# Performance work log

Measured on AMD Instinct MI355X. Metric: run time of the kernel, lower is better.

## Reference

```python
import jax, jax.numpy as jnp
import numpy as np

N_NODES = 100000
N_EDGES = 1600000
IN_CH = 128
HID = 128
N_REL = 8


def setup_inputs() -> dict:
    key = jax.random.key(0)
    k_x, k_src, k_dst, k_et, k_w, k_root, k_b = jax.random.split(key, 7)
    x = jax.random.normal(k_x, (N_NODES, IN_CH), dtype=jnp.float32)
    src = jax.random.randint(k_src, (N_EDGES,), 0, N_NODES)
    dst = jax.random.randint(k_dst, (N_EDGES,), 0, N_NODES)
    edge_index = jnp.stack([src, dst], axis=0)  # [2, E]
    edge_type = jax.random.randint(k_et, (N_EDGES,), 0, N_REL)
    # RGCNConv parameters: per-relation weight, root (self-loop) weight, bias
    scale = 1.0 / np.sqrt(IN_CH)
    W = jax.random.normal(k_w, (N_REL, IN_CH, HID), dtype=jnp.float32) * scale
    root = jax.random.normal(k_root, (IN_CH, HID), dtype=jnp.float32) * scale
    bias = jnp.zeros((HID,), dtype=jnp.float32)
    return {"x": x, "edge_index": edge_index, "edge_type": edge_type,
            "W": W, "root": root, "bias": bias}


def reference(x, edge_index, edge_type, W, root, bias):
    # RGCNConv (mean aggregation per relation) + ReLU. Dropout is identity (eval mode).
    # Aggregate-then-transform: mathematically identical to PyG's
    # transform-then-aggregate since the relation transform is linear,
    # but far cheaper (R matmuls over N nodes instead of E edges).
    N = x.shape[0]
    n_rel = W.shape[0]
    src, dst = edge_index[0], edge_index[1]
    x_src = x[src]  # [E, C] gathered neighbor features
    out = x @ root + bias  # root / self-loop term
    for r in range(n_rel):
        mask = (edge_type == r)
        xm = jnp.where(mask[:, None], x_src, 0.0)  # zero out other relations
        agg = jax.ops.segment_sum(xm, dst, num_segments=N)  # [N, C]
        cnt = jax.ops.segment_sum(mask.astype(x.dtype), dst, num_segments=N)
        mean_agg = agg / jnp.maximum(cnt, 1.0)[:, None]
        out = out + mean_agg @ W[r]
    return jax.nn.relu(out)
```

## Files before the change

kernel.cpp:

```cpp
#include <hip/hip_runtime.h>

#define NREL 8
#define CH   128
#define YW   1152
#define YWD  (YW / 2)
#define NCB  9

#define SCAN_ITEMS   16
#define SCAN_THREADS 256
#define SCAN_CHUNK   (SCAN_ITEMS * SCAN_THREADS)
#define SCAN_SHIFT   12

typedef short  short8v __attribute__((ext_vector_type(8)));
typedef float  f32x4   __attribute__((ext_vector_type(4)));

__device__ __forceinline__ unsigned short f2bf(float f) {
    union { float f; unsigned u; } v; v.f = f;
    return (unsigned short)((v.u + 0x7FFFu + ((v.u >> 16) & 1u)) >> 16);
}
__device__ __forceinline__ float lof(unsigned u) {
    union { unsigned u; float f; } v; v.u = u << 16; return v.f;
}
__device__ __forceinline__ float hif(unsigned u) {
    union { unsigned u; float f; } v; v.u = u & 0xFFFF0000u; return v.f;
}
__device__ __forceinline__ void gload_lds16(const void* g, void* l) {
    __builtin_amdgcn_global_load_lds(
        (const __attribute__((address_space(1))) unsigned int*)g,
        (__attribute__((address_space(3))) unsigned int*)l, 16, 0, 0);
}

__global__ __launch_bounds__(256) void bt2_kernel(
    const float* __restrict__ W, const float* __restrict__ root,
    unsigned short* __restrict__ Bt2)
{
    int idx = blockIdx.x * blockDim.x + threadIdx.x;
    if (idx >= YW * CH) return;
    int rc = idx >> 7, k = idx & 127;
    int r = rc >> 7, c = rc & 127;
    float v = (r < NREL) ? W[(size_t)(r * CH + k) * CH + c]
                         : root[(size_t)k * CH + c];
    Bt2[idx] = f2bf(v);
}

__global__ __launch_bounds__(256) void hist_kernel(
    const int* __restrict__ dst, const int* __restrict__ et,
    int* __restrict__ hist, int E)
{
    int e = blockIdx.x * blockDim.x + threadIdx.x;
    if (e < E) atomicAdd(&hist[dst[e] * NREL + et[e]], 1);
}

__global__ __launch_bounds__(SCAN_THREADS) void scan1_kernel(
    const int* __restrict__ hist, int* __restrict__ ofs,
    int* __restrict__ partials, int S)
{
    __shared__ int lds[SCAN_THREADS];
    int t = threadIdx.x;
    int base = blockIdx.x * SCAN_CHUNK + t * SCAN_ITEMS;
    int v[SCAN_ITEMS];
    int s = 0;
#pragma unroll
    for (int j = 0; j < SCAN_ITEMS; j++) {
        int idx = base + j;
        int h = (idx < S) ? hist[idx] : 0;
        v[j] = s; s += h;
    }
    int run = s;
    lds[t] = run; __syncthreads();
    for (int off = 1; off < SCAN_THREADS; off <<= 1) {
        int y = (t >= off) ? lds[t - off] : 0;
        __syncthreads();
        run += y; lds[t] = run; __syncthreads();
    }
    int tb = run - s;
    if (t == SCAN_THREADS - 1) partials[blockIdx.x] = run;
#pragma unroll
    for (int j = 0; j < SCAN_ITEMS; j++) {
        int idx = base + j;
        if (idx < S) ofs[idx] = tb + v[j];
    }
}

__global__ __launch_bounds__(SCAN_THREADS) void scan2_kernel(
    int* __restrict__ partials, int NB)
{
    __shared__ int lds[SCAN_THREADS];
    int t = threadIdx.x;
    int s = (t < NB) ? partials[t] : 0;
    int run = s;
    lds[t] = run; __syncthreads();
    for (int off = 1; off < SCAN_THREADS; off <<= 1) {
        int y = (t >= off) ? lds[t - off] : 0;
        __syncthreads();
        run += y; lds[t] = run; __syncthreads();
    }
    if (t < NB) partials[t] = run - s;
}

__global__ __launch_bounds__(256) void finalize_kernel(
    int* __restrict__ ofs, const int* __restrict__ partials,
    int* __restrict__ pad_offs, int S)
{
    int i = blockIdx.x * blockDim.x + threadIdx.x;
    if (i < S) ofs[i] += partials[i >> SCAN_SHIFT];
    if (i == 0) pad_offs[0] = 0;
}

__global__ __launch_bounds__(512) void ygemm_fill_kernel(
    const float* __restrict__ x,
    const unsigned short* __restrict__ Bt2,
    unsigned short* __restrict__ y,
    int N,
    const int* __restrict__ src, const int* __restrict__ dst,
    const int* __restrict__ et, int* __restrict__ ofs,
    int* __restrict__ perm, int E, int epb)
{
    __shared__ __align__(16) unsigned short As[128 * 128];
    __shared__ __align__(16) unsigned short Bs[128 * 128];

    int tid  = threadIdx.x;
    int lane = tid & 63;
    int wid  = tid >> 6;
    int wm   = wid >> 2;
    int wn   = wid & 3;
    int r15  = lane & 15;
    int kg   = lane >> 4;
    int n0   = blockIdx.x * 128;

    int eb   = blockIdx.x * epb;
    int elim = eb + epb; if (elim > E) elim = E;
    int p0 = -1, p1 = -1, p2 = -1, p3 = -1;
    int s0 = 0, s1 = 0, s2 = 0, s3 = 0;
    {
        int e0 = eb + tid;
        int e1 = e0 + 512, e2 = e1 + 512, e3 = e2 + 512;
        if (e0 < elim) { s0 = src[e0]; p0 = atomicAdd(&ofs[dst[e0] * NREL + et[e0]], 1); }
        if (e1 < elim) { s1 = src[e1]; p1 = atomicAdd(&ofs[dst[e1] * NREL + et[e1]], 1); }
        if (e2 < elim) { s2 = src[e2]; p2 = atomicAdd(&ofs[dst[e2] * NREL + et[e2]], 1); }
        if (e3 < elim) { s3 = src[e3]; p3 = atomicAdd(&ofs[dst[e3] * NREL + et[e3]], 1); }
    }

    {
        int row = tid >> 2;
        int kq  = tid & 3;
        int gn  = n0 + row; if (gn >= N) gn = N - 1;
        const float* xp = x + (size_t)gn * CH + kq * 32;
#pragma unroll
        for (int s8 = 0; s8 < 4; ++s8) {
            float4 f0 = *(const float4*)(xp + s8 * 8);
            float4 f1 = *(const float4*)(xp + s8 * 8 + 4);
            uint4 v;
            v.x = f2bf(f0.x) | ((unsigned)f2bf(f0.y) << 16);
            v.y = f2bf(f0.z) | ((unsigned)f2bf(f0.w) << 16);
            v.z = f2bf(f1.x) | ((unsigned)f2bf(f1.y) << 16);
            v.w = f2bf(f1.z) | ((unsigned)f2bf(f1.w) << 16);
            int slot = kq * 4 + s8;
            int phys = slot ^ (row & 15);
            *(uint4*)&As[row * 128 + phys * 8] = v;
        }
    }

    if (p0 >= 0) perm[p0] = s0;
    if (p1 >= 0) perm[p1] = s1;
    if (p2 >= 0) perm[p2] = s2;
    if (p3 >= 0) perm[p3] = s3;

    for (int cb = 0; cb < NCB; ++cb) {
#pragma unroll
        for (int i = 0; i < 4; ++i) {
            int chunk = wid * 4 + i;
            int col   = chunk * 4 + (lane >> 4);
            int slog  = (lane & 15) ^ (col & 15);
            const char* srcp = (const char*)(Bt2 + (size_t)(cb * CH + col) * CH + slog * 8);
            gload_lds16(srcp, &Bs[chunk * 512]);
        }
        __syncthreads();

        f32x4 acc[4][2];
#pragma unroll
        for (int i = 0; i < 4; i++)
#pragma unroll
            for (int j = 0; j < 2; j++)
                acc[i][j] = f32x4{0.f, 0.f, 0.f, 0.f};

#pragma unroll
        for (int ks = 0; ks < 4; ++ks) {
            short8v a[4], b[2];
#pragma unroll
            for (int mr = 0; mr < 4; ++mr) {
                int row  = wm * 64 + mr * 16 + r15;
                int phys = (ks * 4 + kg) ^ (row & 15);
                a[mr] = *(const short8v*)&As[row * 128 + phys * 8];
            }
#pragma unroll
            for (int nc = 0; nc < 2; ++nc) {
                int col  = wn * 32 + nc * 16 + r15;
                int phys = (ks * 4 + kg) ^ (col & 15);
                b[nc] = *(const short8v*)&Bs[col * 128 + phys * 8];
            }
#pragma unroll
            for (int mr = 0; mr < 4; ++mr)
#pragma unroll
                for (int nc = 0; nc < 2; ++nc)
                    acc[mr][nc] = __builtin_amdgcn_mfma_f32_16x16x32_bf16(
                        a[mr], b[nc], acc[mr][nc], 0, 0, 0);
        }

#pragma unroll
        for (int mr = 0; mr < 4; ++mr) {
#pragma unroll
            for (int reg = 0; reg < 4; ++reg) {
                int gr = n0 + wm * 64 + mr * 16 + kg * 4 + reg;
                if (gr >= N) continue;
#pragma unroll
                for (int nc = 0; nc < 2; ++nc) {
                    int gc = cb * CH + wn * 32 + nc * 16 + r15;
                    y[(size_t)gr * YW + gc] = f2bf(acc[mr][nc][reg]);
                }
            }
        }
        __syncthreads();
    }
}

__global__ __launch_bounds__(256) void gather_kernel(
    const unsigned short* __restrict__ y,
    const int* __restrict__ perm,
    const int* __restrict__ pad_offs,
    const float* __restrict__ bias,
    float* __restrict__ out, int N)
{
    int wid  = threadIdx.x >> 6;
    int lane = threadIdx.x & 63;
    int n    = blockIdx.x * 4 + wid;
    if (n >= N) return;

    const int* bp = pad_offs + n * NREL;
    int b0 = bp[0], b1 = bp[1], b2 = bp[2], b3 = bp[3], b4 = bp[4];
    int b5 = bp[5], b6 = bp[6], b7 = bp[7], b8 = bp[8];

    const unsigned* y32 = (const unsigned*)y;
    float a0 = 0.f, a1 = 0.f;

    for (int blk = b0; blk < b8; blk += 64) {
        int m = b8 - blk; if (m > 64) m = 64;
        int   pv = 0;
        float wv = 0.f;
        if (lane < m) {
            int g   = blk + lane;
            int s   = perm[g];
            int c1 = g >= b1, c2 = g >= b2, c3 = g >= b3, c4 = g >= b4;
            int c5 = g >= b5, c6 = g >= b6, c7 = g >= b7;
            int r  = c1 + c2 + c3 + c4 + c5 + c6 + c7;
            int br  = b0;
            br  = c1 ? b1 : br;  br  = c2 ? b2 : br;  br  = c3 ? b3 : br;
            br  = c4 ? b4 : br;  br  = c5 ? b5 : br;  br  = c6 ? b6 : br;
            br  = c7 ? b7 : br;
            int br1 = b1;
            br1 = c1 ? b2 : br1; br1 = c2 ? b3 : br1; br1 = c3 ? b4 : br1;
            br1 = c4 ? b5 : br1; br1 = c5 ? b6 : br1; br1 = c6 ? b7 : br1;
            br1 = c7 ? b8 : br1;
            pv = s * 9 + r;
            wv = 1.0f / (float)(br1 - br);
        }

        int j = 0;
#define EDGE_LOAD(K) \
            int   p##K = __shfl(pv, j + K);                     \
            float w##K = __shfl(wv, j + K);                     \
            unsigned u##K = y32[(size_t)p##K * 64 + lane];
#define EDGE_ACC(K) \
            a0 += w##K * lof(u##K); a1 += w##K * hif(u##K);

        for (; j + 16 <= m; j += 16) {
            EDGE_LOAD(0) EDGE_LOAD(1) EDGE_LOAD(2)  EDGE_LOAD(3)
            EDGE_LOAD(4) EDGE_LOAD(5) EDGE_LOAD(6)  EDGE_LOAD(7)
            EDGE_LOAD(8) EDGE_LOAD(9) EDGE_LOAD(10) EDGE_LOAD(11)
            EDGE_LOAD(12) EDGE_LOAD(13) EDGE_LOAD(14) EDGE_LOAD(15)
            EDGE_ACC(0)  EDGE_ACC(1)  EDGE_ACC(2)  EDGE_ACC(3)
            EDGE_ACC(4)  EDGE_ACC(5)  EDGE_ACC(6)  EDGE_ACC(7)
            EDGE_ACC(8)  EDGE_ACC(9)  EDGE_ACC(10) EDGE_ACC(11)
            EDGE_ACC(12) EDGE_ACC(13) EDGE_ACC(14) EDGE_ACC(15)
        }
        if (j + 8 <= m) {
            EDGE_LOAD(0) EDGE_LOAD(1) EDGE_LOAD(2) EDGE_LOAD(3)
            EDGE_LOAD(4) EDGE_LOAD(5) EDGE_LOAD(6) EDGE_LOAD(7)
            EDGE_ACC(0) EDGE_ACC(1) EDGE_ACC(2) EDGE_ACC(3)
            EDGE_ACC(4) EDGE_ACC(5) EDGE_ACC(6) EDGE_ACC(7)
            j += 8;
        }
        if (j + 4 <= m) {
            EDGE_LOAD(0) EDGE_LOAD(1) EDGE_LOAD(2) EDGE_LOAD(3)
            EDGE_ACC(0) EDGE_ACC(1) EDGE_ACC(2) EDGE_ACC(3)
            j += 4;
        }
        for (; j < m; ++j) {
            EDGE_LOAD(0)
            EDGE_ACC(0)
        }
#undef EDGE_LOAD
#undef EDGE_ACC
    }

    unsigned ur = y32[(size_t)n * YWD + (NREL * CH / 2) + lane];
    float o0 = a0 + lof(ur) + bias[lane * 2];
    float o1 = a1 + hif(ur) + bias[lane * 2 + 1];
    float2 ov;
    ov.x = fmaxf(o0, 0.f);
    ov.y = fmaxf(o1, 0.f);
    *(float2*)(out + (size_t)n * CH + lane * 2) = ov;
}

extern "C" void kernel_launch(void* const* d_in, const int* in_sizes, int n_in,
                              void* d_out, int out_size, void* d_ws, size_t ws_size,
                              hipStream_t stream)
{
    const float* x    = (const float*)d_in[0];
    const int*   ei   = (const int*)d_in[1];
    const int*   et   = (const int*)d_in[2];
    const float* W    = (const float*)d_in[3];
    const float* root = (const float*)d_in[4];
    const float* bias = (const float*)d_in[5];
    float*       out  = (float*)d_out;

    int N = in_sizes[0] / CH;
    int E = in_sizes[2];
    const int* src = ei;
    const int* dst = ei + E;

    int S  = N * NREL;
    int NB = (S + SCAN_CHUNK - 1) / SCAN_CHUNK;

    unsigned short* y   = (unsigned short*)d_ws;
    unsigned short* Bt2 = y + (size_t)N * YW;
    int* hist     = (int*)(Bt2 + (size_t)YW * CH);
    int* pad_offs = hist + S;
    int* partials = pad_offs + S + 1;
    int* perm     = partials + 256;
    int* ofs      = pad_offs + 1;

    hipMemsetAsync(hist, 0, (size_t)S * sizeof(int), stream);

    int egrid = (E + 255) / 256;
    int G     = (N + 127) / 128;
    int epb   = ((E + G - 1) / G + 511) & ~511;

    bt2_kernel<<<(YW * CH + 255) / 256, 256, 0, stream>>>(W, root, Bt2);
    hist_kernel<<<egrid, 256, 0, stream>>>(dst, et, hist, E);
    scan1_kernel<<<NB, SCAN_THREADS, 0, stream>>>(hist, ofs, partials, S);
    scan2_kernel<<<1, SCAN_THREADS, 0, stream>>>(partials, NB);
    finalize_kernel<<<(S + 255) / 256, 256, 0, stream>>>(ofs, partials, pad_offs, S);
    ygemm_fill_kernel<<<G, 512, 0, stream>>>(x, Bt2, y, N,
                                             src, dst, et, ofs, perm, E, epb);
    gather_kernel<<<(N + 3) / 4, 256, 0, stream>>>(y, perm, pad_offs, bias, out, N);
}
```

Measured before the change: 318.1 us.

## Switch edge sort to per-node CSR with relation packed into permutation

Edges are now bucketed per destination node instead of per (node, relation). The relation id is packed into the low bits of each perm entry, and the gather reads per-relation mean weights straight from the histogram. This removes the eight-boundary compare/select chain in the gather and shrinks the prefix scan from N*8 to N entries. The GEMM is also retiled to 64-column B chunks (18 passes, one B fragment per wave) with a launch-bounds occupancy hint. The cost is more atomic contention per node counter, plus twice as many GEMM passes, each doing less work.

```diff
diff --git a/kernel.cpp b/kernel.cpp
--- a/kernel.cpp
+++ b/kernel.cpp
@@ -4,12 +4,12 @@
 #define CH   128
 #define YW   1152
 #define YWD  (YW / 2)
-#define NCB  9
-
-#define SCAN_ITEMS   16
+#define NCB2 18
+
 #define SCAN_THREADS 256
-#define SCAN_CHUNK   (SCAN_ITEMS * SCAN_THREADS)
-#define SCAN_SHIFT   12
+#define NSC_ITEMS    4
+#define NSC_CHUNK    1024
+#define NSC_SHIFT    10
 
 typedef short  short8v __attribute__((ext_vector_type(8)));
 typedef float  f32x4   __attribute__((ext_vector_type(4)));
@@ -52,19 +52,24 @@
 }
 
 __global__ __launch_bounds__(SCAN_THREADS) void scan1_kernel(
-    const int* __restrict__ hist, int* __restrict__ ofs,
-    int* __restrict__ partials, int S)
+    const int* __restrict__ hist, int* __restrict__ nofs,
+    int* __restrict__ partials, int N)
 {
     __shared__ int lds[SCAN_THREADS];
     int t = threadIdx.x;
-    int base = blockIdx.x * SCAN_CHUNK + t * SCAN_ITEMS;
-    int v[SCAN_ITEMS];
+    int base = blockIdx.x * NSC_CHUNK + t * NSC_ITEMS;
+    int v[NSC_ITEMS];
     int s = 0;
 #pragma unroll
-    for (int j = 0; j < SCAN_ITEMS; j++) {
-        int idx = base + j;
-        int h = (idx < S) ? hist[idx] : 0;
-        v[j] = s; s += h;
+    for (int j = 0; j < NSC_ITEMS; j++) {
+        int n = base + j;
+        int deg = 0;
+        if (n < N) {
+            int4 a = *(const int4*)(hist + (size_t)n * NREL);
+            int4 b = *(const int4*)(hist + (size_t)n * NREL + 4);
+            deg = a.x + a.y + a.z + a.w + b.x + b.y + b.z + b.w;
+        }
+        v[j] = s; s += deg;
     }
     int run = s;
     lds[t] = run; __syncthreads();
@@ -76,9 +81,9 @@
     int tb = run - s;
     if (t == SCAN_THREADS - 1) partials[blockIdx.x] = run;
 #pragma unroll
-    for (int j = 0; j < SCAN_ITEMS; j++) {
-        int idx = base + j;
-        if (idx < S) ofs[idx] = tb + v[j];
+    for (int j = 0; j < NSC_ITEMS; j++) {
+        int n = base + j;
+        if (n < N) nofs[n] = tb + v[j];
     }
 }
 
@@ -99,25 +104,25 @@
 }
 
 __global__ __launch_bounds__(256) void finalize_kernel(
-    int* __restrict__ ofs, const int* __restrict__ partials,
-    int* __restrict__ pad_offs, int S)
+    int* __restrict__ nofs, const int* __restrict__ partials,
+    int* __restrict__ pad_noffs, int N)
 {
     int i = blockIdx.x * blockDim.x + threadIdx.x;
-    if (i < S) ofs[i] += partials[i >> SCAN_SHIFT];
-    if (i == 0) pad_offs[0] = 0;
-}
-
-__global__ __launch_bounds__(512) void ygemm_fill_kernel(
+    if (i < N) nofs[i] += partials[i >> NSC_SHIFT];
+    if (i == 0) pad_noffs[0] = 0;
+}
+
+__global__ __launch_bounds__(512, 6) void ygemm_fill_kernel(
     const float* __restrict__ x,
     const unsigned short* __restrict__ Bt2,
     unsigned short* __restrict__ y,
     int N,
     const int* __restrict__ src, const int* __restrict__ dst,
-    const int* __restrict__ et, int* __restrict__ ofs,
+    const int* __restrict__ et, int* __restrict__ nofs,
     int* __restrict__ perm, int E, int epb)
 {
     __shared__ __align__(16) unsigned short As[128 * 128];
-    __shared__ __align__(16) unsigned short Bs[128 * 128];
+    __shared__ __align__(16) unsigned short Bs[64 * 128];
 
     int tid  = threadIdx.x;
     int lane = tid & 63;
@@ -131,14 +136,14 @@
     int eb   = blockIdx.x * epb;
     int elim = eb + epb; if (elim > E) elim = E;
     int p0 = -1, p1 = -1, p2 = -1, p3 = -1;
-    int s0 = 0, s1 = 0, s2 = 0, s3 = 0;
+    int v0 = 0, v1 = 0, v2 = 0, v3 = 0;
     {
         int e0 = eb + tid;
         int e1 = e0 + 512, e2 = e1 + 512, e3 = e2 + 512;
-        if (e0 < elim) { s0 = src[e0]; p0 = atomicAdd(&ofs[dst[e0] * NREL + et[e0]], 1); }
-        if (e1 < elim) { s1 = src[e1]; p1 = atomicAdd(&ofs[dst[e1] * NREL + et[e1]], 1); }
-        if (e2 < elim) { s2 = src[e2]; p2 = atomicAdd(&ofs[dst[e2] * NREL + et[e2]], 1); }
-        if (e3 < elim) { s3 = src[e3]; p3 = atomicAdd(&ofs[dst[e3] * NREL + et[e3]], 1); }
+        if (e0 < elim) { v0 = (src[e0] << 3) | et[e0]; p0 = atomicAdd(&nofs[dst[e0]], 1); }
+        if (e1 < elim) { v1 = (src[e1] << 3) | et[e1]; p1 = atomicAdd(&nofs[dst[e1]], 1); }
+        if (e2 < elim) { v2 = (src[e2] << 3) | et[e2]; p2 = atomicAdd(&nofs[dst[e2]], 1); }
+        if (e3 < elim) { v3 = (src[e3] << 3) | et[e3]; p3 = atomicAdd(&nofs[dst[e3]], 1); }
     }
 
     {
@@ -161,50 +166,44 @@
         }
     }
 
-    if (p0 >= 0) perm[p0] = s0;
-    if (p1 >= 0) perm[p1] = s1;
-    if (p2 >= 0) perm[p2] = s2;
-    if (p3 >= 0) perm[p3] = s3;
-
-    for (int cb = 0; cb < NCB; ++cb) {
-#pragma unroll
-        for (int i = 0; i < 4; ++i) {
-            int chunk = wid * 4 + i;
+    if (p0 >= 0) perm[p0] = v0;
+    if (p1 >= 0) perm[p1] = v1;
+    if (p2 >= 0) perm[p2] = v2;
+    if (p3 >= 0) perm[p3] = v3;
+
+    for (int cb = 0; cb < NCB2; ++cb) {
+#pragma unroll
+        for (int i = 0; i < 2; ++i) {
+            int chunk = wid * 2 + i;
             int col   = chunk * 4 + (lane >> 4);
-            int slog  = (lane & 15) ^ (col & 15);
-            const char* srcp = (const char*)(Bt2 + (size_t)(cb * CH + col) * CH + slog * 8);
+            int slot  = (lane & 15) ^ (col & 15);
+            const char* srcp = (const char*)(Bt2 + (size_t)(cb * 64 + col) * CH + slot * 8);
             gload_lds16(srcp, &Bs[chunk * 512]);
         }
         __syncthreads();
 
-        f32x4 acc[4][2];
-#pragma unroll
-        for (int i = 0; i < 4; i++)
-#pragma unroll
-            for (int j = 0; j < 2; j++)
-                acc[i][j] = f32x4{0.f, 0.f, 0.f, 0.f};
+        f32x4 acc[4];
+#pragma unroll
+        for (int i = 0; i < 4; i++) acc[i] = f32x4{0.f, 0.f, 0.f, 0.f};
 
 #pragma unroll
         for (int ks = 0; ks < 4; ++ks) {
-            short8v a[4], b[2];
+            short8v a[4], b;
 #pragma unroll
             for (int mr = 0; mr < 4; ++mr) {
                 int row  = wm * 64 + mr * 16 + r15;
                 int phys = (ks * 4 + kg) ^ (row & 15);
                 a[mr] = *(const short8v*)&As[row * 128 + phys * 8];
             }
-#pragma unroll
-            for (int nc = 0; nc < 2; ++nc) {
-                int col  = wn * 32 + nc * 16 + r15;
+            {
+                int col  = wn * 16 + r15;
                 int phys = (ks * 4 + kg) ^ (col & 15);
-                b[nc] = *(const short8v*)&Bs[col * 128 + phys * 8];
+                b = *(const short8v*)&Bs[col * 128 + phys * 8];
             }
 #pragma unroll
             for (int mr = 0; mr < 4; ++mr)
-#pragma unroll
-                for (int nc = 0; nc < 2; ++nc)
-                    acc[mr][nc] = __builtin_amdgcn_mfma_f32_16x16x32_bf16(
-                        a[mr], b[nc], acc[mr][nc], 0, 0, 0);
+                acc[mr] = __builtin_amdgcn_mfma_f32_16x16x32_bf16(
+                    a[mr], b, acc[mr], 0, 0, 0);
         }
 
 #pragma unroll
@@ -213,11 +212,8 @@
             for (int reg = 0; reg < 4; ++reg) {
                 int gr = n0 + wm * 64 + mr * 16 + kg * 4 + reg;
                 if (gr >= N) continue;
-#pragma unroll
-                for (int nc = 0; nc < 2; ++nc) {
-                    int gc = cb * CH + wn * 32 + nc * 16 + r15;
-                    y[(size_t)gr * YW + gc] = f2bf(acc[mr][nc][reg]);
-                }
+                int gc = cb * 64 + wn * 16 + r15;
+                y[(size_t)gr * YW + gc] = f2bf(acc[mr][reg]);
             }
         }
         __syncthreads();
@@ -227,7 +223,8 @@
 __global__ __launch_bounds__(256) void gather_kernel(
     const unsigned short* __restrict__ y,
     const int* __restrict__ perm,
-    const int* __restrict__ pad_offs,
+    const int* __restrict__ pad_noffs,
+    const int* __restrict__ hist,
     const float* __restrict__ bias,
     float* __restrict__ out, int N)
 {
@@ -236,38 +233,43 @@
     int n    = blockIdx.x * 4 + wid;
     if (n >= N) return;
 
-    const int* bp = pad_offs + n * NREL;
-    int b0 = bp[0], b1 = bp[1], b2 = bp[2], b3 = bp[3], b4 = bp[4];
-    int b5 = bp[5], b6 = bp[6], b7 = bp[7], b8 = bp[8];
+    int beg = pad_noffs[n];
+    int end = pad_noffs[n + 1];
+
+    int4 h0 = *(const int4*)(hist + (size_t)n * NREL);
+    int4 h1 = *(const int4*)(hist + (size_t)n * NREL + 4);
+    float iw0 = 1.0f / (float)max(h0.x, 1);
+    float iw1 = 1.0f / (float)max(h0.y, 1);
+    float iw2 = 1.0f / (float)max(h0.z, 1);
+    float iw3 = 1.0f / (float)max(h0.w, 1);
+    float iw4 = 1.0f / (float)max(h1.x, 1);
+    float iw5 = 1.0f / (float)max(h1.y, 1);
+    float iw6 = 1.0f / (float)max(h1.z, 1);
+    float iw7 = 1.0f / (float)max(h1.w, 1);
 
     const unsigned* y32 = (const unsigned*)y;
     float a0 = 0.f, a1 = 0.f;
 
-    for (int blk = b0; blk < b8; blk += 64) {
-        int m = b8 - blk; if (m > 64) m = 64;
-        int   pv = 0;
+    for (int blk = beg; blk < end; blk += 64) {
+        int m = end - blk; if (m > 64) m = 64;
+        int   rv = 0;
         float wv = 0.f;
         if (lane < m) {
-            int g   = blk + lane;
-            int s   = perm[g];
-            int c1 = g >= b1, c2 = g >= b2, c3 = g >= b3, c4 = g >= b4;
-            int c5 = g >= b5, c6 = g >= b6, c7 = g >= b7;
-            int r  = c1 + c2 + c3 + c4 + c5 + c6 + c7;
-            int br  = b0;
-            br  = c1 ? b1 : br;  br  = c2 ? b2 : br;  br  = c3 ? b3 : br;
-            br  = c4 ? b4 : br;  br  = c5 ? b5 : br;  br  = c6 ? b6 : br;
-            br  = c7 ? b7 : br;
-            int br1 = b1;
-            br1 = c1 ? b2 : br1; br1 = c2 ? b3 : br1; br1 = c3 ? b4 : br1;
-            br1 = c4 ? b5 : br1; br1 = c5 ? b6 : br1; br1 = c6 ? b7 : br1;
-            br1 = c7 ? b8 : br1;
-            pv = s * 9 + r;
-            wv = 1.0f / (float)(br1 - br);
+            int pv  = perm[blk + lane];
+            int rel = pv & 7;
+            rv = pv + (pv >> 3);
+            float wa = (rel & 1) ? iw1 : iw0;
+            float wb = (rel & 1) ? iw3 : iw2;
+            float wc = (rel & 1) ? iw5 : iw4;
+            float wd = (rel & 1) ? iw7 : iw6;
+            float we_ = (rel & 2) ? wb : wa;
+            float wf  = (rel & 2) ? wd : wc;
+            wv = (rel & 4) ? wf : we_;
         }
 
         int j = 0;
 #define EDGE_LOAD(K) \
-            int   p##K = __shfl(pv, j + K);                     \
+            int   p##K = __shfl(rv, j + K);                     \
             float w##K = __shfl(wv, j + K);                     \
             unsigned u##K = y32[(size_t)p##K * 64 + lane];
 #define EDGE_ACC(K) \
@@ -329,29 +331,29 @@
     const int* src = ei;
     const int* dst = ei + E;
 
-    int S  = N * NREL;
-    int NB = (S + SCAN_CHUNK - 1) / SCAN_CHUNK;
+    int S   = N * NREL;
+    int NBn = (N + NSC_CHUNK - 1) / NSC_CHUNK;
 
     unsigned short* y   = (unsigned short*)d_ws;
     unsigned short* Bt2 = y + (size_t)N * YW;
-    int* hist     = (int*)(Bt2 + (size_t)YW * CH);
-    int* pad_offs = hist + S;
-    int* partials = pad_offs + S + 1;
-    int* perm     = partials + 256;
-    int* ofs      = pad_offs + 1;
+    int* hist      = (int*)(Bt2 + (size_t)YW * CH);
+    int* pad_noffs = hist + S;
+    int* partials  = pad_noffs + N + 1;
+    int* perm      = partials + 256;
+    int* nofs      = pad_noffs + 1;
 
     hipMemsetAsync(hist, 0, (size_t)S * sizeof(int), stream);
 
     int egrid = (E + 255) / 256;
     int G     = (N + 127) / 128;
-    int epb   = ((E + G - 1) / G + 511) & ~511;
+    int epb   = ((E + G - 1) / G + 2047) & ~2047;
 
     bt2_kernel<<<(YW * CH + 255) / 256, 256, 0, stream>>>(W, root, Bt2);
     hist_kernel<<<egrid, 256, 0, stream>>>(dst, et, hist, E);
-    scan1_kernel<<<NB, SCAN_THREADS, 0, stream>>>(hist, ofs, partials, S);
-    scan2_kernel<<<1, SCAN_THREADS, 0, stream>>>(partials, NB);
-    finalize_kernel<<<(S + 255) / 256, 256, 0, stream>>>(ofs, partials, pad_offs, S);
+    scan1_kernel<<<NBn, SCAN_THREADS, 0, stream>>>(hist, nofs, partials, N);
+    scan2_kernel<<<1, SCAN_THREADS, 0, stream>>>(partials, NBn);
+    finalize_kernel<<<(N + 255) / 256, 256, 0, stream>>>(nofs, partials, pad_noffs, N);
     ygemm_fill_kernel<<<G, 512, 0, stream>>>(x, Bt2, y, N,
-                                             src, dst, et, ofs, perm, E, epb);
-    gather_kernel<<<(N + 3) / 4, 256, 0, stream>>>(y, perm, pad_offs, bias, out, N);
-}
+                                             src, dst, et, nofs, perm, E, epb);
+    gather_kernel<<<(N + 3) / 4, 256, 0, stream>>>(y, perm, pad_noffs, hist, bias, out, N);
+}
```

Result: no change. 313.3 us (-1.5%).
